# Optimization experiments

Hardware: AMD Instinct MI355X
Metric: run time of the kernel (lower is better)

Reference implementation:

```python
import jax, jax.numpy as jnp
import numpy as np

STRIDE = 32
WINDOW = 16


def setup_inputs() -> dict:
    key = jax.random.key(0)
    kq, kk, kv = jax.random.split(key, 3)
    B, H, S, D = 1, 16, 2048, 64
    q = jax.random.normal(kq, (B, H, S, D), dtype=jnp.float32)
    k = jax.random.normal(kk, (B, H, S, D), dtype=jnp.float32)
    v = jax.random.normal(kv, (B, H, S, D), dtype=jnp.float32)
    return {"q": q, "k": k, "v": v}


def _strided_attention(q, k, v, stride=STRIDE, w=WINDOW):
    b, h, n, d = q.shape
    scale = jnp.asarray(1.0 / np.sqrt(d), dtype=q.dtype)

    # strided (global) tokens: indices 0, stride, 2*stride, ...  [S_str]
    str_idx = jnp.arange(0, n, stride)
    k_str = k[:, :, str_idx, :]  # [b,h,S_str,d]
    v_str = v[:, :, str_idx, :]

    # local window gather: token i attends to j in [i-w, i+w]  (L = 2w+1 slots)
    offs = jnp.arange(-w, w + 1)                      # [L]
    pos = jnp.arange(n)[:, None] + offs[None, :]      # [n, L]
    local_valid = (pos >= 0) & (pos < n)              # [n, L]
    pos_c = jnp.clip(pos, 0, n - 1)
    k_loc = k[:, :, pos_c, :]                         # [b,h,n,L,d]
    v_loc = v[:, :, pos_c, :]                         # [b,h,n,L,d]

    # In the original, strided keys are concatenated ONLY when start > 0,
    # i.e. when i > w (since strided_indices[0] == 0 is inside the window
    # whenever start == 0). Duplicates (strided token inside the local
    # window) are intentionally kept, matching torch.cat semantics.
    use_str = jnp.arange(n) > w                       # [n]

    sc_loc = jnp.einsum('bhnd,bhnld->bhnl', q, k_loc) * scale
    sc_loc = jnp.where(local_valid[None, None], sc_loc, -jnp.inf)
    sc_str = jnp.einsum('bhnd,bhsd->bhns', q, k_str) * scale
    sc_str = jnp.where(use_str[None, None, :, None], sc_str, -jnp.inf)

    L = offs.shape[0]
    attn = jax.nn.softmax(jnp.concatenate([sc_loc, sc_str], axis=-1), axis=-1)
    attn = jnp.nan_to_num(attn, nan=0.0)
    a_loc, a_str = attn[..., :L], attn[..., L:]

    out = jnp.einsum('bhnl,bhnld->bhnd', a_loc, v_loc) \
        + jnp.einsum('bhns,bhsd->bhnd', a_str, v_str)
    return out


def reference(q, k, v):
    return _strided_attention(q, k, v)
```

## Files before the change

kernel.cpp:

```cpp
#include <hip/hip_runtime.h>
#include <math.h>


typedef __attribute__((ext_vector_type(8))) short bf16x8;
typedef __attribute__((ext_vector_type(4))) float f32x4;

constexpr int H = 16, S = 2048, D = 64, W = 16;
constexpr int QB   = 64;
constexpr int NLOC = 96;
constexpr int NROWS = 160;
constexpr int NT   = 10;
constexpr float S2 = 0.18033688011112042f;

constexpr int KSTRIDE = 72;
constexpr int VSTR    = 168;
constexpr int KB      = 0;
constexpr int VTB     = NROWS * KSTRIDE;
constexpr int LDS_U   = VTB + D * VSTR;

__device__ __forceinline__ ushort f2bf(float x) {
    union { float f; unsigned u; } t; t.f = x;
    unsigned r = t.u + 0x7fffu + ((t.u >> 16) & 1u);
    return (ushort)(r >> 16);
}
__device__ __forceinline__ float bf2f(ushort b) {
    union { float f; unsigned u; } t; t.u = ((unsigned)b) << 16;
    return t.f;
}
__device__ __forceinline__ unsigned pk2(float a, float b) {
    return (unsigned)f2bf(a) | ((unsigned)f2bf(b) << 16);
}
__device__ __forceinline__ bf16x8 cvt8(const float4& a, const float4& b) {
    union { bf16x8 v; unsigned u[4]; } r;
    r.u[0] = pk2(a.x, a.y); r.u[1] = pk2(a.z, a.w);
    r.u[2] = pk2(b.x, b.y); r.u[3] = pk2(b.z, b.w);
    return r.v;
}
__device__ __forceinline__ void cvt_hilo(const float4& a, const float4& b,
                                         bf16x8& hi, bf16x8& lo) {
    const float xs[8] = {a.x, a.y, a.z, a.w, b.x, b.y, b.z, b.w};
    union { bf16x8 v; ushort u[8]; } Hv, Lv;
#pragma unroll
    for (int j = 0; j < 8; ++j) {
        const ushort hb = f2bf(xs[j]);
        Hv.u[j] = hb;
        Lv.u[j] = f2bf(xs[j] - bf2f(hb));
    }
    hi = Hv.v; lo = Lv.v;
}
__device__ __forceinline__ int rowpos(int r, int n0) {
    if (r < NLOC) {
        int p = n0 - W + r;
        return p < 0 ? 0 : (p > S - 1 ? S - 1 : p);
    }
    return (r - NLOC) * 32;
}

__global__ __launch_bounds__(256, 2) void strided_attn_mfma(
    const float* __restrict__ q,
    const float* __restrict__ k,
    const float* __restrict__ v,
    float* __restrict__ out)
{
    __shared__ ushort lds[LDS_U];

    const int tid  = threadIdx.x;
    const int w    = tid >> 6;
    const int lane = tid & 63;
    const int c    = lane & 15;
    const int g    = lane >> 4;
    const int bid  = blockIdx.x;
    const int swz  = (bid & 7) * 64 + (bid >> 3);
    const int h    = swz >> 5;
    const int n0   = (swz & 31) << 6;

    const float* __restrict__ qh = q + (size_t)(h * S) * D;
    const float* __restrict__ kh = k + (size_t)(h * S) * D;
    const float* __restrict__ vh = v + (size_t)(h * S) * D;

    const int ntask = (tid < 128) ? 3 : 2;
    float4 vreg[3][4];
#pragma unroll
    for (int tt = 0; tt < 3; ++tt) {
        if (tt < ntask) {
            const int tau = tid + (tt << 8);
            const int rp = tau % 80, ch = tau / 80;
            const float* s0 = vh + (size_t)rowpos(2 * rp,     n0) * D + ch * 8;
            const float* s1 = vh + (size_t)rowpos(2 * rp + 1, n0) * D + ch * 8;
            vreg[tt][0] = *(const float4*)s0;
            vreg[tt][1] = *(const float4*)(s0 + 4);
            vreg[tt][2] = *(const float4*)s1;
            vreg[tt][3] = *(const float4*)(s1 + 4);
        }
    }

    const int qb = w * 16;
    const int qi = qb + c;
    const int nq = n0 + qi;
    const float* qrow = qh + (size_t)(n0 + qb + c) * D;
    const float4 qv00 = *(const float4*)(qrow + g * 8);
    const float4 qv01 = *(const float4*)(qrow + g * 8 + 4);
    const float4 qv10 = *(const float4*)(qrow + 32 + g * 8);
    const float4 qv11 = *(const float4*)(qrow + 32 + g * 8 + 4);

    for (int t = tid; t < 1280; t += 256) {
        const int row = t >> 3, ch = t & 7;
        const float* src = kh + (size_t)rowpos(row, n0) * D + ch * 8;
        const float4 a = *(const float4*)src;
        const float4 b = *(const float4*)(src + 4);
        *(bf16x8*)&lds[KB + row * KSTRIDE + ch * 8] = cvt8(a, b);
    }

    bf16x8 bQH0, bQL0, bQH1, bQL1;
    cvt_hilo(qv00, qv01, bQH0, bQL0);
    cvt_hilo(qv10, qv11, bQH1, bQL1);

#pragma unroll
    for (int tt = 0; tt < 3; ++tt) {
        if (tt < ntask) {
            const int tau = tid + (tt << 8);
            const int rp = tau % 80, ch = tau / 80;
            const float r0[8] = {vreg[tt][0].x, vreg[tt][0].y, vreg[tt][0].z, vreg[tt][0].w,
                                 vreg[tt][1].x, vreg[tt][1].y, vreg[tt][1].z, vreg[tt][1].w};
            const float r1[8] = {vreg[tt][2].x, vreg[tt][2].y, vreg[tt][2].z, vreg[tt][2].w,
                                 vreg[tt][3].x, vreg[tt][3].y, vreg[tt][3].z, vreg[tt][3].w};
            const int kk = 2 * rp;
            const int kt = kk >> 5, rem = kk & 31;
            const int slot = kt * 32 + ((rem >> 2) & 3) * 8 + (rem >> 4) * 4 + (rem & 3);
#pragma unroll
            for (int j = 0; j < 8; ++j)
                *(unsigned*)&lds[VTB + (ch * 8 + j) * VSTR + slot] = pk2(r0[j], r1[j]);
        }
    }

    __syncthreads();

    f32x4 acc[NT];
#pragma unroll
    for (int t = 0; t < NT; ++t) acc[t] = (f32x4){0.f, 0.f, 0.f, 0.f};
#pragma unroll
    for (int t = 0; t < NT; ++t) {
        const int kb = KB + (t * 16 + c) * KSTRIDE + g * 8;
        const bf16x8 a0 = *(bf16x8*)&lds[kb];
        const bf16x8 a1 = *(bf16x8*)&lds[kb + 32];
        f32x4 a4 = acc[t];
        a4 = __builtin_amdgcn_mfma_f32_16x16x32_bf16(a0, bQH0, a4, 0, 0, 0);
        a4 = __builtin_amdgcn_mfma_f32_16x16x32_bf16(a1, bQH1, a4, 0, 0, 0);
        a4 = __builtin_amdgcn_mfma_f32_16x16x32_bf16(a0, bQL0, a4, 0, 0, 0);
        a4 = __builtin_amdgcn_mfma_f32_16x16x32_bf16(a1, bQL1, a4, 0, 0, 0);
        acc[t] = a4;
    }

    float p[NT][4];
#pragma unroll
    for (int t = 0; t < 6; ++t) {
#pragma unroll
        for (int i = 0; i < 4; ++i) {
            const int j = t * 16 + 4 * g + i;
            const bool ok = ((unsigned)(j - qi) <= 32u) &&
                            ((unsigned)(n0 - W + j) < (unsigned)S);
            p[t][i] = ok ? acc[t][i] * S2 : -INFINITY;
        }
    }
    const bool us = nq > W;
#pragma unroll
    for (int t = 6; t < NT; ++t)
#pragma unroll
        for (int i = 0; i < 4; ++i)
            p[t][i] = us ? acc[t][i] * S2 : -INFINITY;

    float m = -INFINITY;
#pragma unroll
    for (int t = 0; t < NT; ++t)
#pragma unroll
        for (int i = 0; i < 4; ++i) m = fmaxf(m, p[t][i]);
    m = fmaxf(m, __shfl_xor(m, 16));
    m = fmaxf(m, __shfl_xor(m, 32));

    float l = 0.f;
#pragma unroll
    for (int t = 0; t < NT; ++t)
#pragma unroll
        for (int i = 0; i < 4; ++i) { p[t][i] = exp2f(p[t][i] - m); l += p[t][i]; }
    l += __shfl_xor(l, 16);
    l += __shfl_xor(l, 32);
    const float inv = 1.0f / l;

    union { bf16x8 v; unsigned u[4]; } pa[5];
#pragma unroll
    for (int kt = 0; kt < 5; ++kt) {
        pa[kt].u[0] = pk2(p[2 * kt][0] * inv,     p[2 * kt][1] * inv);
        pa[kt].u[1] = pk2(p[2 * kt][2] * inv,     p[2 * kt][3] * inv);
        pa[kt].u[2] = pk2(p[2 * kt + 1][0] * inv, p[2 * kt + 1][1] * inv);
        pa[kt].u[3] = pk2(p[2 * kt + 1][2] * inv, p[2 * kt + 1][3] * inv);
    }

    f32x4 o[4];
#pragma unroll
    for (int dt = 0; dt < 4; ++dt) o[dt] = (f32x4){0.f, 0.f, 0.f, 0.f};
#pragma unroll
    for (int kt = 0; kt < 5; ++kt) {
#pragma unroll
        for (int dt = 0; dt < 4; ++dt) {
            const bf16x8 vb = *(bf16x8*)&lds[VTB + (dt * 16 + c) * VSTR + kt * 32 + g * 8];
            o[dt] = __builtin_amdgcn_mfma_f32_16x16x32_bf16(pa[kt].v, vb, o[dt], 0, 0, 0);
        }
    }

#pragma unroll
    for (int i = 0; i < 4; ++i) {
        const int n = n0 + qb + 4 * g + i;
        float* op = out + ((size_t)(h * S) + n) * D + c;
#pragma unroll
        for (int dt = 0; dt < 4; ++dt) op[dt * 16] = o[dt][i];
    }
}

extern "C" void kernel_launch(void* const* d_in, const int* in_sizes, int n_in,
                              void* d_out, int out_size, void* d_ws, size_t ws_size,
                              hipStream_t stream) {
    (void)in_sizes; (void)n_in; (void)d_ws; (void)ws_size; (void)out_size;
    const float* q = (const float*)d_in[0];
    const float* k = (const float*)d_in[1];
    const float* v = (const float*)d_in[2];
    float* out     = (float*)d_out;

    dim3 grid(H * (S / QB));
    dim3 block(256);
    strided_attn_mfma<<<grid, block, 0, stream>>>(q, k, v, out);
}
```

Measured before the change: 16.37 us.

## Double query block to 128 rows and alias V-transpose LDS over K buffer

Each block now handles 128 queries with 512 threads, so the halo and strided K/V rows are loaded once per 128 queries instead of once per 64. LDS is reused: K occupies it for QK^T, and after a barrier the transposed V is written into the same space, with V held packed in registers until then. The softmax scale is folded into Q before the hi/lo split, and the score array is computed in place in the accumulators. The grid halves to 256 blocks and per-thread register pressure rises, which may reduce parallelism on a GPU with many CUs.

```diff
diff --git a/kernel.cpp b/kernel.cpp
--- a/kernel.cpp
+++ b/kernel.cpp
@@ -6,17 +6,18 @@
 typedef __attribute__((ext_vector_type(4))) float f32x4;
 
 constexpr int H = 16, S = 2048, D = 64, W = 16;
-constexpr int QB   = 64;
-constexpr int NLOC = 96;
-constexpr int NROWS = 160;
-constexpr int NT   = 10;
+constexpr int QB    = 128;
+constexpr int NLOC  = 160;
+constexpr int NROWS = 224;
+constexpr int NT    = 14;
+constexpr int NLT   = 10;
 constexpr float S2 = 0.18033688011112042f;
 
 constexpr int KSTRIDE = 72;
-constexpr int VSTR    = 168;
+constexpr int VSTR    = 232;
 constexpr int KB      = 0;
-constexpr int VTB     = NROWS * KSTRIDE;
-constexpr int LDS_U   = VTB + D * VSTR;
+constexpr int VTB     = 0;
+constexpr int LDS_U   = NROWS * KSTRIDE;
 
 __device__ __forceinline__ ushort f2bf(float x) {
     union { float f; unsigned u; } t; t.f = x;
@@ -56,7 +57,7 @@
     return (r - NLOC) * 32;
 }
 
-__global__ __launch_bounds__(256, 2) void strided_attn_mfma(
+__global__ __launch_bounds__(512, 2) void strided_attn_mfma(
     const float* __restrict__ q,
     const float* __restrict__ k,
     const float* __restrict__ v,
@@ -70,21 +71,23 @@
     const int c    = lane & 15;
     const int g    = lane >> 4;
     const int bid  = blockIdx.x;
-    const int swz  = (bid & 7) * 64 + (bid >> 3);
-    const int h    = swz >> 5;
-    const int n0   = (swz & 31) << 6;
+    const int swz  = (bid & 7) * 32 + (bid >> 3);
+    const int h    = swz >> 4;
+    const int n0   = (swz & 15) << 7;
 
     const float* __restrict__ qh = q + (size_t)(h * S) * D;
     const float* __restrict__ kh = k + (size_t)(h * S) * D;
     const float* __restrict__ vh = v + (size_t)(h * S) * D;
 
-    const int ntask = (tid < 128) ? 3 : 2;
-    float4 vreg[3][4];
-#pragma unroll
-    for (int tt = 0; tt < 3; ++tt) {
+    const int ntask = (tid < 384) ? 2 : 1;
+    float4 vreg[2][4];
+    int vrp[2], vch[2];
+#pragma unroll
+    for (int tt = 0; tt < 2; ++tt) {
         if (tt < ntask) {
-            const int tau = tid + (tt << 8);
-            const int rp = tau % 80, ch = tau / 80;
+            const int tau = tid + (tt << 9);
+            const int rp = tau % 112, ch = tau / 112;
+            vrp[tt] = rp; vch[tt] = ch;
             const float* s0 = vh + (size_t)rowpos(2 * rp,     n0) * D + ch * 8;
             const float* s1 = vh + (size_t)rowpos(2 * rp + 1, n0) * D + ch * 8;
             vreg[tt][0] = *(const float4*)s0;
@@ -98,12 +101,12 @@
     const int qi = qb + c;
     const int nq = n0 + qi;
     const float* qrow = qh + (size_t)(n0 + qb + c) * D;
-    const float4 qv00 = *(const float4*)(qrow + g * 8);
-    const float4 qv01 = *(const float4*)(qrow + g * 8 + 4);
-    const float4 qv10 = *(const float4*)(qrow + 32 + g * 8);
-    const float4 qv11 = *(const float4*)(qrow + 32 + g * 8 + 4);
-
-    for (int t = tid; t < 1280; t += 256) {
+    float4 qv00 = *(const float4*)(qrow + g * 8);
+    float4 qv01 = *(const float4*)(qrow + g * 8 + 4);
+    float4 qv10 = *(const float4*)(qrow + 32 + g * 8);
+    float4 qv11 = *(const float4*)(qrow + 32 + g * 8 + 4);
+
+    for (int t = tid; t < 1792; t += 512) {
         const int row = t >> 3, ch = t & 7;
         const float* src = kh + (size_t)rowpos(row, n0) * D + ch * 8;
         const float4 a = *(const float4*)src;
@@ -111,28 +114,26 @@
         *(bf16x8*)&lds[KB + row * KSTRIDE + ch * 8] = cvt8(a, b);
     }
 
+    qv00.x *= S2; qv00.y *= S2; qv00.z *= S2; qv00.w *= S2;
+    qv01.x *= S2; qv01.y *= S2; qv01.z *= S2; qv01.w *= S2;
+    qv10.x *= S2; qv10.y *= S2; qv10.z *= S2; qv10.w *= S2;
+    qv11.x *= S2; qv11.y *= S2; qv11.z *= S2; qv11.w *= S2;
     bf16x8 bQH0, bQL0, bQH1, bQL1;
     cvt_hilo(qv00, qv01, bQH0, bQL0);
     cvt_hilo(qv10, qv11, bQH1, bQL1);
 
-#pragma unroll
-    for (int tt = 0; tt < 3; ++tt) {
+    unsigned vpk[2][8];
+#pragma unroll
+    for (int tt = 0; tt < 2; ++tt) {
         if (tt < ntask) {
-            const int tau = tid + (tt << 8);
-            const int rp = tau % 80, ch = tau / 80;
             const float r0[8] = {vreg[tt][0].x, vreg[tt][0].y, vreg[tt][0].z, vreg[tt][0].w,
                                  vreg[tt][1].x, vreg[tt][1].y, vreg[tt][1].z, vreg[tt][1].w};
             const float r1[8] = {vreg[tt][2].x, vreg[tt][2].y, vreg[tt][2].z, vreg[tt][2].w,
                                  vreg[tt][3].x, vreg[tt][3].y, vreg[tt][3].z, vreg[tt][3].w};
-            const int kk = 2 * rp;
-            const int kt = kk >> 5, rem = kk & 31;
-            const int slot = kt * 32 + ((rem >> 2) & 3) * 8 + (rem >> 4) * 4 + (rem & 3);
-#pragma unroll
-            for (int j = 0; j < 8; ++j)
-                *(unsigned*)&lds[VTB + (ch * 8 + j) * VSTR + slot] = pk2(r0[j], r1[j]);
-        }
-    }
-
+#pragma unroll
+            for (int j = 0; j < 8; ++j) vpk[tt][j] = pk2(r0[j], r1[j]);
+        }
+    }
     __syncthreads();
 
     f32x4 acc[NT];
@@ -151,29 +152,28 @@
         acc[t] = a4;
     }
 
-    float p[NT][4];
-#pragma unroll
-    for (int t = 0; t < 6; ++t) {
+#pragma unroll
+    for (int t = 0; t < NLT; ++t) {
 #pragma unroll
         for (int i = 0; i < 4; ++i) {
             const int j = t * 16 + 4 * g + i;
             const bool ok = ((unsigned)(j - qi) <= 32u) &&
                             ((unsigned)(n0 - W + j) < (unsigned)S);
-            p[t][i] = ok ? acc[t][i] * S2 : -INFINITY;
+            acc[t][i] = ok ? acc[t][i] : -INFINITY;
         }
     }
     const bool us = nq > W;
 #pragma unroll
-    for (int t = 6; t < NT; ++t)
+    for (int t = NLT; t < NT; ++t)
 #pragma unroll
         for (int i = 0; i < 4; ++i)
-            p[t][i] = us ? acc[t][i] * S2 : -INFINITY;
+            acc[t][i] = us ? acc[t][i] : -INFINITY;
 
     float m = -INFINITY;
 #pragma unroll
     for (int t = 0; t < NT; ++t)
 #pragma unroll
-        for (int i = 0; i < 4; ++i) m = fmaxf(m, p[t][i]);
+        for (int i = 0; i < 4; ++i) m = fmaxf(m, acc[t][i]);
     m = fmaxf(m, __shfl_xor(m, 16));
     m = fmaxf(m, __shfl_xor(m, 32));
 
@@ -181,25 +181,41 @@
 #pragma unroll
     for (int t = 0; t < NT; ++t)
 #pragma unroll
-        for (int i = 0; i < 4; ++i) { p[t][i] = exp2f(p[t][i] - m); l += p[t][i]; }
+        for (int i = 0; i < 4; ++i) { acc[t][i] = exp2f(acc[t][i] - m); l += acc[t][i]; }
     l += __shfl_xor(l, 16);
     l += __shfl_xor(l, 32);
     const float inv = 1.0f / l;
 
-    union { bf16x8 v; unsigned u[4]; } pa[5];
-#pragma unroll
-    for (int kt = 0; kt < 5; ++kt) {
-        pa[kt].u[0] = pk2(p[2 * kt][0] * inv,     p[2 * kt][1] * inv);
-        pa[kt].u[1] = pk2(p[2 * kt][2] * inv,     p[2 * kt][3] * inv);
-        pa[kt].u[2] = pk2(p[2 * kt + 1][0] * inv, p[2 * kt + 1][1] * inv);
-        pa[kt].u[3] = pk2(p[2 * kt + 1][2] * inv, p[2 * kt + 1][3] * inv);
-    }
+    union { bf16x8 v; unsigned u[4]; } pa[7];
+#pragma unroll
+    for (int kt = 0; kt < 7; ++kt) {
+        pa[kt].u[0] = pk2(acc[2 * kt][0] * inv,     acc[2 * kt][1] * inv);
+        pa[kt].u[1] = pk2(acc[2 * kt][2] * inv,     acc[2 * kt][3] * inv);
+        pa[kt].u[2] = pk2(acc[2 * kt + 1][0] * inv, acc[2 * kt + 1][1] * inv);
+        pa[kt].u[3] = pk2(acc[2 * kt + 1][2] * inv, acc[2 * kt + 1][3] * inv);
+    }
+
+    __syncthreads();
+
+#pragma unroll
+    for (int tt = 0; tt < 2; ++tt) {
+        if (tt < ntask) {
+            const int rp = vrp[tt], ch = vch[tt];
+            const int kk = 2 * rp;
+            const int kt = kk >> 5, rem = kk & 31;
+            const int slot = kt * 32 + ((rem >> 2) & 3) * 8 + (rem >> 4) * 4 + (rem & 3);
+#pragma unroll
+            for (int j = 0; j < 8; ++j)
+                *(unsigned*)&lds[VTB + (ch * 8 + j) * VSTR + slot] = vpk[tt][j];
+        }
+    }
+    __syncthreads();
 
     f32x4 o[4];
 #pragma unroll
     for (int dt = 0; dt < 4; ++dt) o[dt] = (f32x4){0.f, 0.f, 0.f, 0.f};
 #pragma unroll
-    for (int kt = 0; kt < 5; ++kt) {
+    for (int kt = 0; kt < 7; ++kt) {
 #pragma unroll
         for (int dt = 0; dt < 4; ++dt) {
             const bf16x8 vb = *(bf16x8*)&lds[VTB + (dt * 16 + c) * VSTR + kt * 32 + g * 8];
@@ -226,6 +242,6 @@
     float* out     = (float*)d_out;
 
     dim3 grid(H * (S / QB));
-    dim3 block(256);
+    dim3 block(512);
     strided_attn_mfma<<<grid, block, 0, stream>>>(q, k, v, out);
 }
```

New measurement: 16.46 us. No clear change (+0.5%).

## Process two query tiles per block with reused LDS regions and prefetched loads

Applied to the files above, without the earlier changes.

Each block now handles two 64-query tiles instead of one, halving the grid. All global loads for both tiles (V, Q, K) are issued up front, and two LDS regions are reused in turns: K tile then transposed V, with the second tile's staging overlapping the first tile's compute. The softmax scale is folded into Q before the hi/lo split, which removes a per-score multiply. The cost is higher register pressure (launch bounds occupancy drops to 1), more barriers and fewer blocks, which may leave CUs underused.

```diff
diff --git a/kernel.cpp b/kernel.cpp
--- a/kernel.cpp
+++ b/kernel.cpp
@@ -8,15 +8,13 @@
 constexpr int H = 16, S = 2048, D = 64, W = 16;
 constexpr int QB   = 64;
 constexpr int NLOC = 96;
-constexpr int NROWS = 160;
 constexpr int NT   = 10;
 constexpr float S2 = 0.18033688011112042f;
 
 constexpr int KSTRIDE = 72;
 constexpr int VSTR    = 168;
-constexpr int KB      = 0;
-constexpr int VTB     = NROWS * KSTRIDE;
-constexpr int LDS_U   = VTB + D * VSTR;
+constexpr int REG     = 160 * KSTRIDE;
+constexpr int LDS_U   = 2 * REG;
 
 __device__ __forceinline__ ushort f2bf(float x) {
     union { float f; unsigned u; } t; t.f = x;
@@ -36,9 +34,9 @@
     r.u[2] = pk2(b.x, b.y); r.u[3] = pk2(b.z, b.w);
     return r.v;
 }
-__device__ __forceinline__ void cvt_hilo(const float4& a, const float4& b,
-                                         bf16x8& hi, bf16x8& lo) {
-    const float xs[8] = {a.x, a.y, a.z, a.w, b.x, b.y, b.z, b.w};
+__device__ __forceinline__ void cvt_hilo(float4 a, float4 b, bf16x8& hi, bf16x8& lo) {
+    const float xs[8] = {a.x * S2, a.y * S2, a.z * S2, a.w * S2,
+                         b.x * S2, b.y * S2, b.z * S2, b.w * S2};
     union { bf16x8 v; ushort u[8]; } Hv, Lv;
 #pragma unroll
     for (int j = 0; j < 8; ++j) {
@@ -48,21 +46,131 @@
     }
     hi = Hv.v; lo = Lv.v;
 }
-__device__ __forceinline__ int rowpos(int r, int n0) {
+__device__ __forceinline__ int rowpos(int r, int m0) {
     if (r < NLOC) {
-        int p = n0 - W + r;
+        int p = m0 - W + r;
         return p < 0 ? 0 : (p > S - 1 ? S - 1 : p);
     }
     return (r - NLOC) * 32;
 }
 
-__global__ __launch_bounds__(256, 2) void strided_attn_mfma(
+__device__ __forceinline__ void tile_qk_softmax(
+    const ushort* __restrict__ kb,
+    const bf16x8 qh0, const bf16x8 qh1, const bf16x8 ql0, const bf16x8 ql1,
+    const int c, const int g, const int qi, const int m0, bf16x8 pa[5])
+{
+    f32x4 acc[NT];
+#pragma unroll
+    for (int t = 0; t < NT; ++t) acc[t] = (f32x4){0.f, 0.f, 0.f, 0.f};
+#pragma unroll
+    for (int t = 0; t < NT; ++t) {
+        const bf16x8 a0 = *(const bf16x8*)&kb[(t * 16 + c) * KSTRIDE + g * 8];
+        const bf16x8 a1 = *(const bf16x8*)&kb[(t * 16 + c) * KSTRIDE + g * 8 + 32];
+        f32x4 a4 = acc[t];
+        a4 = __builtin_amdgcn_mfma_f32_16x16x32_bf16(a0, qh0, a4, 0, 0, 0);
+        a4 = __builtin_amdgcn_mfma_f32_16x16x32_bf16(a1, qh1, a4, 0, 0, 0);
+        a4 = __builtin_amdgcn_mfma_f32_16x16x32_bf16(a0, ql0, a4, 0, 0, 0);
+        a4 = __builtin_amdgcn_mfma_f32_16x16x32_bf16(a1, ql1, a4, 0, 0, 0);
+        acc[t] = a4;
+    }
+#pragma unroll
+    for (int t = 0; t < 6; ++t) {
+#pragma unroll
+        for (int i = 0; i < 4; ++i) {
+            const int j = t * 16 + 4 * g + i;
+            const bool ok = ((unsigned)(j - qi) <= 32u) &&
+                            ((unsigned)(m0 - W + j) < (unsigned)S);
+            acc[t][i] = ok ? acc[t][i] : -INFINITY;
+        }
+    }
+    const bool us = (m0 + qi) > W;
+#pragma unroll
+    for (int t = 6; t < NT; ++t)
+#pragma unroll
+        for (int i = 0; i < 4; ++i)
+            acc[t][i] = us ? acc[t][i] : -INFINITY;
+
+    float m = -INFINITY;
+#pragma unroll
+    for (int t = 0; t < NT; ++t)
+#pragma unroll
+        for (int i = 0; i < 4; ++i) m = fmaxf(m, acc[t][i]);
+    m = fmaxf(m, __shfl_xor(m, 16));
+    m = fmaxf(m, __shfl_xor(m, 32));
+
+    float l = 0.f;
+#pragma unroll
+    for (int t = 0; t < NT; ++t)
+#pragma unroll
+        for (int i = 0; i < 4; ++i) { acc[t][i] = exp2f(acc[t][i] - m); l += acc[t][i]; }
+    l += __shfl_xor(l, 16);
+    l += __shfl_xor(l, 32);
+    const float inv = 1.0f / l;
+
+    union { bf16x8 v; unsigned u[4]; } pk;
+#pragma unroll
+    for (int kt = 0; kt < 5; ++kt) {
+        pk.u[0] = pk2(acc[2 * kt][0] * inv,     acc[2 * kt][1] * inv);
+        pk.u[1] = pk2(acc[2 * kt][2] * inv,     acc[2 * kt][3] * inv);
+        pk.u[2] = pk2(acc[2 * kt + 1][0] * inv, acc[2 * kt + 1][1] * inv);
+        pk.u[3] = pk2(acc[2 * kt + 1][2] * inv, acc[2 * kt + 1][3] * inv);
+        pa[kt] = pk.v;
+    }
+}
+
+__device__ __forceinline__ void vt_write(ushort* __restrict__ vtb,
+                                         const unsigned vpk[3][8],
+                                         const int ntask, const int tid)
+{
+#pragma unroll
+    for (int tt = 0; tt < 3; ++tt) {
+        if (tt < ntask) {
+            const int tau = tid + (tt << 8);
+            const int rp = tau % 80, ch = tau / 80;
+            const int kk = 2 * rp;
+            const int kt = kk >> 5, rem = kk & 31;
+            const int slot = kt * 32 + ((rem >> 2) & 3) * 8 + (rem >> 4) * 4 + (rem & 3);
+#pragma unroll
+            for (int j = 0; j < 8; ++j)
+                *(unsigned*)&vtb[(ch * 8 + j) * VSTR + slot] = vpk[tt][j];
+        }
+    }
+}
+
+__device__ __forceinline__ void tile_pv_store(
+    const ushort* __restrict__ vtb, const bf16x8 pa[5],
+    const int c, const int g, const int qb, const int m0,
+    float* __restrict__ outh)
+{
+    f32x4 o[4];
+#pragma unroll
+    for (int dt = 0; dt < 4; ++dt) o[dt] = (f32x4){0.f, 0.f, 0.f, 0.f};
+#pragma unroll
+    for (int kt = 0; kt < 5; ++kt) {
+#pragma unroll
+        for (int dt = 0; dt < 4; ++dt) {
+            const bf16x8 vb = *(const bf16x8*)&vtb[(dt * 16 + c) * VSTR + kt * 32 + g * 8];
+            o[dt] = __builtin_amdgcn_mfma_f32_16x16x32_bf16(pa[kt], vb, o[dt], 0, 0, 0);
+        }
+    }
+#pragma unroll
+    for (int i = 0; i < 4; ++i) {
+        const int n = m0 + qb + 4 * g + i;
+        float* op = outh + (size_t)n * D + c;
+#pragma unroll
+        for (int dt = 0; dt < 4; ++dt) op[dt * 16] = o[dt][i];
+    }
+}
+
+__global__ __launch_bounds__(256, 1) void strided_attn_mfma(
     const float* __restrict__ q,
     const float* __restrict__ k,
     const float* __restrict__ v,
     float* __restrict__ out)
 {
     __shared__ ushort lds[LDS_U];
+    ushort* Areg = lds;
+    ushort* Breg = lds + REG;
 
     const int tid  = threadIdx.x;
     const int w    = tid >> 6;
@@ -70,150 +178,134 @@
     const int c    = lane & 15;
     const int g    = lane >> 4;
     const int bid  = blockIdx.x;
-    const int swz  = (bid & 7) * 64 + (bid >> 3);
-    const int h    = swz >> 5;
-    const int n0   = (swz & 31) << 6;
+    const int swz  = (bid & 7) * 32 + (bid >> 3);
+    const int h    = swz >> 4;
+    const int n0   = (swz & 15) << 7;
+    const int m0   = n0;
+    const int m1   = n0 + QB;
 
     const float* __restrict__ qh = q + (size_t)(h * S) * D;
     const float* __restrict__ kh = k + (size_t)(h * S) * D;
     const float* __restrict__ vh = v + (size_t)(h * S) * D;
+    float* __restrict__ outh = out + (size_t)(h * S) * D;
 
     const int ntask = (tid < 128) ? 3 : 2;
-    float4 vreg[3][4];
+    const int qb = w * 16;
+    const int qi = qb + c;
+
+    float4 vr0[3][4];
 #pragma unroll
     for (int tt = 0; tt < 3; ++tt) {
         if (tt < ntask) {
             const int tau = tid + (tt << 8);
             const int rp = tau % 80, ch = tau / 80;
-            const float* s0 = vh + (size_t)rowpos(2 * rp,     n0) * D + ch * 8;
-            const float* s1 = vh + (size_t)rowpos(2 * rp + 1, n0) * D + ch * 8;
-            vreg[tt][0] = *(const float4*)s0;
-            vreg[tt][1] = *(const float4*)(s0 + 4);
-            vreg[tt][2] = *(const float4*)s1;
-            vreg[tt][3] = *(const float4*)(s1 + 4);
-        }
-    }
-
-    const int qb = w * 16;
-    const int qi = qb + c;
-    const int nq = n0 + qi;
-    const float* qrow = qh + (size_t)(n0 + qb + c) * D;
-    const float4 qv00 = *(const float4*)(qrow + g * 8);
-    const float4 qv01 = *(const float4*)(qrow + g * 8 + 4);
-    const float4 qv10 = *(const float4*)(qrow + 32 + g * 8);
-    const float4 qv11 = *(const float4*)(qrow + 32 + g * 8 + 4);
-
-    for (int t = tid; t < 1280; t += 256) {
-        const int row = t >> 3, ch = t & 7;
-        const float* src = kh + (size_t)rowpos(row, n0) * D + ch * 8;
-        const float4 a = *(const float4*)src;
-        const float4 b = *(const float4*)(src + 4);
-        *(bf16x8*)&lds[KB + row * KSTRIDE + ch * 8] = cvt8(a, b);
-    }
-
-    bf16x8 bQH0, bQL0, bQH1, bQL1;
-    cvt_hilo(qv00, qv01, bQH0, bQL0);
-    cvt_hilo(qv10, qv11, bQH1, bQL1);
-
+            const float* s0 = vh + (size_t)rowpos(2 * rp,     m0) * D + ch * 8;
+            const float* s1 = vh + (size_t)rowpos(2 * rp + 1, m0) * D + ch * 8;
+            vr0[tt][0] = *(const float4*)s0;
+            vr0[tt][1] = *(const float4*)(s0 + 4);
+            vr0[tt][2] = *(const float4*)s1;
+            vr0[tt][3] = *(const float4*)(s1 + 4);
+        }
+    }
+    const float* q0row = qh + (size_t)(m0 + qb + c) * D;
+    const float4 q0a = *(const float4*)(q0row + g * 8);
+    const float4 q0b = *(const float4*)(q0row + g * 8 + 4);
+    const float4 q0c = *(const float4*)(q0row + 32 + g * 8);
+    const float4 q0d = *(const float4*)(q0row + 32 + g * 8 + 4);
+    const float* q1row = qh + (size_t)(m1 + qb + c) * D;
+    const float4 q1a = *(const float4*)(q1row + g * 8);
+    const float4 q1b = *(const float4*)(q1row + g * 8 + 4);
+    const float4 q1c = *(const float4*)(q1row + 32 + g * 8);
+    const float4 q1d = *(const float4*)(q1row + 32 + g * 8 + 4);
+    float4 vr1[3][4];
 #pragma unroll
     for (int tt = 0; tt < 3; ++tt) {
         if (tt < ntask) {
             const int tau = tid + (tt << 8);
             const int rp = tau % 80, ch = tau / 80;
-            const float r0[8] = {vreg[tt][0].x, vreg[tt][0].y, vreg[tt][0].z, vreg[tt][0].w,
-                                 vreg[tt][1].x, vreg[tt][1].y, vreg[tt][1].z, vreg[tt][1].w};
-            const float r1[8] = {vreg[tt][2].x, vreg[tt][2].y, vreg[tt][2].z, vreg[tt][2].w,
-                                 vreg[tt][3].x, vreg[tt][3].y, vreg[tt][3].z, vreg[tt][3].w};
-            const int kk = 2 * rp;
-            const int kt = kk >> 5, rem = kk & 31;
-            const int slot = kt * 32 + ((rem >> 2) & 3) * 8 + (rem >> 4) * 4 + (rem & 3);
-#pragma unroll
-            for (int j = 0; j < 8; ++j)
-                *(unsigned*)&lds[VTB + (ch * 8 + j) * VSTR + slot] = pk2(r0[j], r1[j]);
-        }
-    }
-
-    __syncthreads();
-
-    f32x4 acc[NT];
-#pragma unroll
-    for (int t = 0; t < NT; ++t) acc[t] = (f32x4){0.f, 0.f, 0.f, 0.f};
-#pragma unroll
-    for (int t = 0; t < NT; ++t) {
-        const int kb = KB + (t * 16 + c) * KSTRIDE + g * 8;
-        const bf16x8 a0 = *(bf16x8*)&lds[kb];
-        const bf16x8 a1 = *(bf16x8*)&lds[kb + 32];
-        f32x4 a4 = acc[t];
-        a4 = __builtin_amdgcn_mfma_f32_16x16x32_bf16(a0, bQH0, a4, 0, 0, 0);
-        a4 = __builtin_amdgcn_mfma_f32_16x16x32_bf16(a1, bQH1, a4, 0, 0, 0);
-        a4 = __builtin_amdgcn_mfma_f32_16x16x32_bf16(a0, bQL0, a4, 0, 0, 0);
-        a4 = __builtin_amdgcn_mfma_f32_16x16x32_bf16(a1, bQL1, a4, 0, 0, 0);
-        acc[t] = a4;
-    }
-
-    float p[NT][4];
-#pragma unroll
-    for (int t = 0; t < 6; ++t) {
-#pragma unroll
-        for (int i = 0; i < 4; ++i) {
-            const int j = t * 16 + 4 * g + i;
-            const bool ok = ((unsigned)(j - qi) <= 32u) &&
-                            ((unsigned)(n0 - W + j) < (unsigned)S);
-            p[t][i] = ok ? acc[t][i] * S2 : -INFINITY;
-        }
-    }
-    const bool us = nq > W;
-#pragma unroll
-    for (int t = 6; t < NT; ++t)
-#pragma unroll
-        for (int i = 0; i < 4; ++i)
-            p[t][i] = us ? acc[t][i] * S2 : -INFINITY;
-
-    float m = -INFINITY;
-#pragma unroll
-    for (int t = 0; t < NT; ++t)
-#pragma unroll
-        for (int i = 0; i < 4; ++i) m = fmaxf(m, p[t][i]);
-    m = fmaxf(m, __shfl_xor(m, 16));
-    m = fmaxf(m, __shfl_xor(m, 32));
-
-    float l = 0.f;
-#pragma unroll
-    for (int t = 0; t < NT; ++t)
-#pragma unroll
-        for (int i = 0; i < 4; ++i) { p[t][i] = exp2f(p[t][i] - m); l += p[t][i]; }
-    l += __shfl_xor(l, 16);
-    l += __shfl_xor(l, 32);
-    const float inv = 1.0f / l;
-
-    union { bf16x8 v; unsigned u[4]; } pa[5];
-#pragma unroll
-    for (int kt = 0; kt < 5; ++kt) {
-        pa[kt].u[0] = pk2(p[2 * kt][0] * inv,     p[2 * kt][1] * inv);
-        pa[kt].u[1] = pk2(p[2 * kt][2] * inv,     p[2 * kt][3] * inv);
-        pa[kt].u[2] = pk2(p[2 * kt + 1][0] * inv, p[2 * kt + 1][1] * inv);
-        pa[kt].u[3] = pk2(p[2 * kt + 1][2] * inv, p[2 * kt + 1][3] * inv);
-    }
-
-    f32x4 o[4];
-#pragma unroll
-    for (int dt = 0; dt < 4; ++dt) o[dt] = (f32x4){0.f, 0.f, 0.f, 0.f};
-#pragma unroll
-    for (int kt = 0; kt < 5; ++kt) {
-#pragma unroll
-        for (int dt = 0; dt < 4; ++dt) {
-            const bf16x8 vb = *(bf16x8*)&lds[VTB + (dt * 16 + c) * VSTR + kt * 32 + g * 8];
-            o[dt] = __builtin_amdgcn_mfma_f32_16x16x32_bf16(pa[kt].v, vb, o[dt], 0, 0, 0);
-        }
-    }
-
-#pragma unroll
-    for (int i = 0; i < 4; ++i) {
-        const int n = n0 + qb + 4 * g + i;
-        float* op = out + ((size_t)(h * S) + n) * D + c;
-#pragma unroll
-        for (int dt = 0; dt < 4; ++dt) op[dt * 16] = o[dt][i];
-    }
+            const float* s0 = vh + (size_t)rowpos(2 * rp,     m1) * D + ch * 8;
+            const float* s1 = vh + (size_t)rowpos(2 * rp + 1, m1) * D + ch * 8;
+            vr1[tt][0] = *(const float4*)s0;
+            vr1[tt][1] = *(const float4*)(s0 + 4);
+            vr1[tt][2] = *(const float4*)s1;
+            vr1[tt][3] = *(const float4*)(s1 + 4);
+        }
+    }
+
+#pragma unroll
+    for (int it = 0; it < 5; ++it) {
+        const int t = tid + (it << 8);
+        const int row = t >> 3, ch = t & 7;
+        const float* src = kh + (size_t)rowpos(row, m0) * D + ch * 8;
+        const float4 a = *(const float4*)src;
+        const float4 b = *(const float4*)(src + 4);
+        *(bf16x8*)&Areg[row * KSTRIDE + ch * 8] = cvt8(a, b);
+    }
+
+    bf16x8 q0h0, q0l0, q0h1, q0l1, q1h0, q1l0, q1h1, q1l1;
+    cvt_hilo(q0a, q0b, q0h0, q0l0);
+    cvt_hilo(q0c, q0d, q0h1, q0l1);
+    cvt_hilo(q1a, q1b, q1h0, q1l0);
+    cvt_hilo(q1c, q1d, q1h1, q1l1);
+
+    unsigned vpk0[3][8], vpk1[3][8];
+#pragma unroll
+    for (int tt = 0; tt < 3; ++tt) {
+        if (tt < ntask) {
+            const float r0[8] = {vr0[tt][0].x, vr0[tt][0].y, vr0[tt][0].z, vr0[tt][0].w,
+                                 vr0[tt][1].x, vr0[tt][1].y, vr0[tt][1].z, vr0[tt][1].w};
+            const float r1[8] = {vr0[tt][2].x, vr0[tt][2].y, vr0[tt][2].z, vr0[tt][2].w,
+                                 vr0[tt][3].x, vr0[tt][3].y, vr0[tt][3].z, vr0[tt][3].w};
+            const float s0[8] = {vr1[tt][0].x, vr1[tt][0].y, vr1[tt][0].z, vr1[tt][0].w,
+                                 vr1[tt][1].x, vr1[tt][1].y, vr1[tt][1].z, vr1[tt][1].w};
+            const float s1[8] = {vr1[tt][2].x, vr1[tt][2].y, vr1[tt][2].z, vr1[tt][2].w,
+                                 vr1[tt][3].x, vr1[tt][3].y, vr1[tt][3].z, vr1[tt][3].w};
+#pragma unroll
+            for (int j = 0; j < 8; ++j) {
+                vpk0[tt][j] = pk2(r0[j], r1[j]);
+                vpk1[tt][j] = pk2(s0[j], s1[j]);
+            }
+        }
+    }
+
+    float4 k1a[5], k1b[5];
+#pragma unroll
+    for (int it = 0; it < 5; ++it) {
+        const int t = tid + (it << 8);
+        const int row = t >> 3, ch = t & 7;
+        const float* src = kh + (size_t)rowpos(row, m1) * D + ch * 8;
+        k1a[it] = *(const float4*)src;
+        k1b[it] = *(const float4*)(src + 4);
+    }
+
+    __syncthreads();
+
+    bf16x8 pa0[5];
+    tile_qk_softmax(Areg, q0h0, q0h1, q0l0, q0l1, c, g, qi, m0, pa0);
+
+    __syncthreads();
+
+    vt_write(Areg, vpk0, ntask, tid);
+#pragma unroll
+    for (int it = 0; it < 5; ++it) {
+        const int t = tid + (it << 8);
+        const int row = t >> 3, ch = t & 7;
+        *(bf16x8*)&Breg[row * KSTRIDE + ch * 8] = cvt8(k1a[it], k1b[it]);
+    }
+
+    __syncthreads();
+
+    tile_pv_store(Areg, pa0, c, g, qb, m0, outh);
+    bf16x8 pa1[5];
+    tile_qk_softmax(Breg, q1h0, q1h1, q1l0, q1l1, c, g, qi, m1, pa1);
+
+    __syncthreads();
+
+    vt_write(Breg, vpk1, ntask, tid);
+
+    __syncthreads();
+
+    tile_pv_store(Breg, pa1, c, g, qb, m1, outh);
 }
 
 extern "C" void kernel_launch(void* const* d_in, const int* in_sizes, int n_in,
@@ -225,7 +317,7 @@
     const float* v = (const float*)d_in[2];
     float* out     = (float*)d_out;
 
-    dim3 grid(H * (S / QB));
+    dim3 grid(H * (S / 128));
     dim3 block(256);
     strided_attn_mfma<<<grid, block, 0, stream>>>(q, k, v, out);
 }
```

Measured after the change: 17.55 us. +7.2%, slower.

## Skip out-of-window key tiles per wave and alias K/V LDS buffers

Applied to the files above, without the earlier changes.

Each wave now computes QK^T only for the three local 16-row key tiles that can intersect its query window, plus the four strided tiles, instead of all ten tiles. PV uses four MFMAs per output tile instead of five, with zero-padded probability fragments chosen by wave parity. K and transposed V share one LDS buffer, which lowers LDS use, at the cost of an extra barrier before V is written. The softmax scale is folded into the Q hi/lo split.

```diff
diff --git a/kernel.cpp b/kernel.cpp
--- a/kernel.cpp
+++ b/kernel.cpp
@@ -8,15 +8,12 @@
 constexpr int H = 16, S = 2048, D = 64, W = 16;
 constexpr int QB   = 64;
 constexpr int NLOC = 96;
-constexpr int NROWS = 160;
-constexpr int NT   = 10;
+constexpr int NRT  = 7;
 constexpr float S2 = 0.18033688011112042f;
 
 constexpr int KSTRIDE = 72;
 constexpr int VSTR    = 168;
-constexpr int KB      = 0;
-constexpr int VTB     = NROWS * KSTRIDE;
-constexpr int LDS_U   = VTB + D * VSTR;
+constexpr int LDS_U   = 160 * KSTRIDE;
 
 __device__ __forceinline__ ushort f2bf(float x) {
     union { float f; unsigned u; } t; t.f = x;
@@ -36,9 +33,9 @@
     r.u[2] = pk2(b.x, b.y); r.u[3] = pk2(b.z, b.w);
     return r.v;
 }
-__device__ __forceinline__ void cvt_hilo(const float4& a, const float4& b,
-                                         bf16x8& hi, bf16x8& lo) {
-    const float xs[8] = {a.x, a.y, a.z, a.w, b.x, b.y, b.z, b.w};
+__device__ __forceinline__ void cvt_hilo(float4 a, float4 b, bf16x8& hi, bf16x8& lo) {
+    const float xs[8] = {a.x * S2, a.y * S2, a.z * S2, a.w * S2,
+                         b.x * S2, b.y * S2, b.z * S2, b.w * S2};
     union { bf16x8 v; ushort u[8]; } Hv, Lv;
 #pragma unroll
     for (int j = 0; j < 8; ++j) {
@@ -103,17 +100,103 @@
     const float4 qv10 = *(const float4*)(qrow + 32 + g * 8);
     const float4 qv11 = *(const float4*)(qrow + 32 + g * 8 + 4);
 
-    for (int t = tid; t < 1280; t += 256) {
+#pragma unroll
+    for (int it = 0; it < 5; ++it) {
+        const int t = tid + (it << 8);
         const int row = t >> 3, ch = t & 7;
         const float* src = kh + (size_t)rowpos(row, n0) * D + ch * 8;
         const float4 a = *(const float4*)src;
         const float4 b = *(const float4*)(src + 4);
-        *(bf16x8*)&lds[KB + row * KSTRIDE + ch * 8] = cvt8(a, b);
+        *(bf16x8*)&lds[row * KSTRIDE + ch * 8] = cvt8(a, b);
     }
 
     bf16x8 bQH0, bQL0, bQH1, bQL1;
     cvt_hilo(qv00, qv01, bQH0, bQL0);
     cvt_hilo(qv10, qv11, bQH1, bQL1);
+
+    __syncthreads();
+
+    f32x4 acc[NRT];
+#pragma unroll
+    for (int t = 0; t < NRT; ++t) acc[t] = (f32x4){0.f, 0.f, 0.f, 0.f};
+#pragma unroll
+    for (int t = 0; t < NRT; ++t) {
+        const int gt = (t < 3) ? (w + t) : (t + 3);
+        const int kb = (gt * 16 + c) * KSTRIDE + g * 8;
+        const bf16x8 a0 = *(const bf16x8*)&lds[kb];
+        const bf16x8 a1 = *(const bf16x8*)&lds[kb + 32];
+        f32x4 a4 = acc[t];
+        a4 = __builtin_amdgcn_mfma_f32_16x16x32_bf16(a0, bQH0, a4, 0, 0, 0);
+        a4 = __builtin_amdgcn_mfma_f32_16x16x32_bf16(a1, bQH1, a4, 0, 0, 0);
+        a4 = __builtin_amdgcn_mfma_f32_16x16x32_bf16(a0, bQL0, a4, 0, 0, 0);
+        a4 = __builtin_amdgcn_mfma_f32_16x16x32_bf16(a1, bQL1, a4, 0, 0, 0);
+        acc[t] = a4;
+    }
+
+#pragma unroll
+    for (int t = 0; t < 3; ++t) {
+#pragma unroll
+        for (int i = 0; i < 4; ++i) {
+            const int j = (w + t) * 16 + 4 * g + i;
+            const bool ok = ((unsigned)(j - qi) <= 32u) &&
+                            ((unsigned)(n0 - W + j) < (unsigned)S);
+            acc[t][i] = ok ? acc[t][i] : -INFINITY;
+        }
+    }
+    const bool us = nq > W;
+#pragma unroll
+    for (int t = 3; t < NRT; ++t)
+#pragma unroll
+        for (int i = 0; i < 4; ++i)
+            acc[t][i] = us ? acc[t][i] : -INFINITY;
+
+    float m = -INFINITY;
+#pragma unroll
+    for (int t = 0; t < NRT; ++t)
+#pragma unroll
+        for (int i = 0; i < 4; ++i) m = fmaxf(m, acc[t][i]);
+    m = fmaxf(m, __shfl_xor(m, 16));
+    m = fmaxf(m, __shfl_xor(m, 32));
+
+    float l = 0.f;
+#pragma unroll
+    for (int t = 0; t < NRT; ++t)
+#pragma unroll
+        for (int i = 0; i < 4; ++i) { acc[t][i] = exp2f(acc[t][i] - m); l += acc[t][i]; }
+    l += __shfl_xor(l, 16);
+    l += __shfl_xor(l, 32);
+    const float inv = 1.0f / l;
+
+    const int klo = w >> 1;
+    const bool even = (w & 1) == 0;
+    union { bf16x8 v; unsigned u[4]; } paL0, paL1, paS0, paS1;
+    if (even) {
+        paL0.u[0] = pk2(acc[0][0] * inv, acc[0][1] * inv);
+        paL0.u[1] = pk2(acc[0][2] * inv, acc[0][3] * inv);
+        paL0.u[2] = pk2(acc[1][0] * inv, acc[1][1] * inv);
+        paL0.u[3] = pk2(acc[1][2] * inv, acc[1][3] * inv);
+        paL1.u[0] = pk2(acc[2][0] * inv, acc[2][1] * inv);
+        paL1.u[1] = pk2(acc[2][2] * inv, acc[2][3] * inv);
+        paL1.u[2] = 0; paL1.u[3] = 0;
+    } else {
+        paL0.u[0] = 0; paL0.u[1] = 0;
+        paL0.u[2] = pk2(acc[0][0] * inv, acc[0][1] * inv);
+        paL0.u[3] = pk2(acc[0][2] * inv, acc[0][3] * inv);
+        paL1.u[0] = pk2(acc[1][0] * inv, acc[1][1] * inv);
+        paL1.u[1] = pk2(acc[1][2] * inv, acc[1][3] * inv);
+        paL1.u[2] = pk2(acc[2][0] * inv, acc[2][1] * inv);
+        paL1.u[3] = pk2(acc[2][2] * inv, acc[2][3] * inv);
+    }
+    paS0.u[0] = pk2(acc[3][0] * inv, acc[3][1] * inv);
+    paS0.u[1] = pk2(acc[3][2] * inv, acc[3][3] * inv);
+    paS0.u[2] = pk2(acc[4][0] * inv, acc[4][1] * inv);
+    paS0.u[3] = pk2(acc[4][2] * inv, acc[4][3] * inv);
+    paS1.u[0] = pk2(acc[5][0] * inv, acc[5][1] * inv);
+    paS1.u[1] = pk2(acc[5][2] * inv, acc[5][3] * inv);
+    paS1.u[2] = pk2(acc[6][0] * inv, acc[6][1] * inv);
+    paS1.u[3] = pk2(acc[6][2] * inv, acc[6][3] * inv);
+
+    __syncthreads();
 
 #pragma unroll
     for (int tt = 0; tt < 3; ++tt) {
@@ -129,82 +212,27 @@
             const int slot = kt * 32 + ((rem >> 2) & 3) * 8 + (rem >> 4) * 4 + (rem & 3);
 #pragma unroll
             for (int j = 0; j < 8; ++j)
-                *(unsigned*)&lds[VTB + (ch * 8 + j) * VSTR + slot] = pk2(r0[j], r1[j]);
+                *(unsigned*)&lds[(ch * 8 + j) * VSTR + slot] = pk2(r0[j], r1[j]);
         }
     }
-
     __syncthreads();
 
-    f32x4 acc[NT];
-#pragma unroll
-    for (int t = 0; t < NT; ++t) acc[t] = (f32x4){0.f, 0.f, 0.f, 0.f};
-#pragma unroll
-    for (int t = 0; t < NT; ++t) {
-        const int kb = KB + (t * 16 + c) * KSTRIDE + g * 8;
-        const bf16x8 a0 = *(bf16x8*)&lds[kb];
-        const bf16x8 a1 = *(bf16x8*)&lds[kb + 32];
-        f32x4 a4 = acc[t];
-        a4 = __builtin_amdgcn_mfma_f32_16x16x32_bf16(a0, bQH0, a4, 0, 0, 0);
-        a4 = __builtin_amdgcn_mfma_f32_16x16x32_bf16(a1, bQH1, a4, 0, 0, 0);
-        a4 = __builtin_amdgcn_mfma_f32_16x16x32_bf16(a0, bQL0, a4, 0, 0, 0);
-        a4 = __builtin_amdgcn_mfma_f32_16x16x32_bf16(a1, bQL1, a4, 0, 0, 0);
-        acc[t] = a4;
-    }
-
-    float p[NT][4];
-#pragma unroll
-    for (int t = 0; t < 6; ++t) {
-#pragma unroll
-        for (int i = 0; i < 4; ++i) {
-            const int j = t * 16 + 4 * g + i;
-            const bool ok = ((unsigned)(j - qi) <= 32u) &&
-                            ((unsigned)(n0 - W + j) < (unsigned)S);
-            p[t][i] = ok ? acc[t][i] * S2 : -INFINITY;
-        }
-    }
-    const bool us = nq > W;
-#pragma unroll
-    for (int t = 6; t < NT; ++t)
-#pragma unroll
-        for (int i = 0; i < 4; ++i)
-            p[t][i] = us ? acc[t][i] * S2 : -INFINITY;
-
-    float m = -INFINITY;
-#pragma unroll
-    for (int t = 0; t < NT; ++t)
-#pragma unroll
-        for (int i = 0; i < 4; ++i) m = fmaxf(m, p[t][i]);
-    m = fmaxf(m, __shfl_xor(m, 16));
-    m = fmaxf(m, __shfl_xor(m, 32));
-
-    float l = 0.f;
-#pragma unroll
-    for (int t = 0; t < NT; ++t)
-#pragma unroll
-        for (int i = 0; i < 4; ++i) { p[t][i] = exp2f(p[t][i] - m); l += p[t][i]; }
-    l += __shfl_xor(l, 16);
-    l += __shfl_xor(l, 32);
-    const float inv = 1.0f / l;
-
-    union { bf16x8 v; unsigned u[4]; } pa[5];
-#pragma unroll
-    for (int kt = 0; kt < 5; ++kt) {
-        pa[kt].u[0] = pk2(p[2 * kt][0] * inv,     p[2 * kt][1] * inv);
-        pa[kt].u[1] = pk2(p[2 * kt][2] * inv,     p[2 * kt][3] * inv);
-        pa[kt].u[2] = pk2(p[2 * kt + 1][0] * inv, p[2 * kt + 1][1] * inv);
-        pa[kt].u[3] = pk2(p[2 * kt + 1][2] * inv, p[2 * kt + 1][3] * inv);
-    }
-
     f32x4 o[4];
 #pragma unroll
     for (int dt = 0; dt < 4; ++dt) o[dt] = (f32x4){0.f, 0.f, 0.f, 0.f};
 #pragma unroll
-    for (int kt = 0; kt < 5; ++kt) {
-#pragma unroll
-        for (int dt = 0; dt < 4; ++dt) {
-            const bf16x8 vb = *(bf16x8*)&lds[VTB + (dt * 16 + c) * VSTR + kt * 32 + g * 8];
-            o[dt] = __builtin_amdgcn_mfma_f32_16x16x32_bf16(pa[kt].v, vb, o[dt], 0, 0, 0);
-        }
+    for (int dt = 0; dt < 4; ++dt) {
+        const int vb = (dt * 16 + c) * VSTR + g * 8;
+        const bf16x8 v0 = *(const bf16x8*)&lds[vb + (klo)     * 32];
+        const bf16x8 v1 = *(const bf16x8*)&lds[vb + (klo + 1) * 32];
+        const bf16x8 v2 = *(const bf16x8*)&lds[vb + 3 * 32];
+        const bf16x8 v3 = *(const bf16x8*)&lds[vb + 4 * 32];
+        f32x4 od = o[dt];
+        od = __builtin_amdgcn_mfma_f32_16x16x32_bf16(paL0.v, v0, od, 0, 0, 0);
+        od = __builtin_amdgcn_mfma_f32_16x16x32_bf16(paL1.v, v1, od, 0, 0, 0);
+        od = __builtin_amdgcn_mfma_f32_16x16x32_bf16(paS0.v, v2, od, 0, 0, 0);
+        od = __builtin_amdgcn_mfma_f32_16x16x32_bf16(paS1.v, v3, od, 0, 0, 0);
+        o[dt] = od;
     }
 
 #pragma unroll
```

New measurement: 15.32 us. 1.07x faster.
